# Optimization experiments

Measured on AMD Instinct MI355X. Metric: run time of the kernel, lower is better.

The kernel has to match this reference:

```python
import jax, jax.numpy as jnp
import numpy as np

N = 100000
E = 1600000
F_IN = 100
H = 64
C = 18
K = 2  # num_stacks
T = 2  # num_layers


def setup_inputs() -> dict:
    key = jax.random.key(0)
    ks = jax.random.split(key, 12)
    def glorot(k, shape):
        fan = shape[-2] + shape[-1]
        s = jnp.sqrt(6.0 / fan)
        return jax.random.uniform(k, shape, jnp.float32, -s, s)
    return {
        "x": jax.random.normal(ks[0], (N, F_IN), jnp.float32),
        "edge_index": jax.random.randint(ks[1], (2, E), 0, N, jnp.int64),
        "init_w1": glorot(ks[2], (K, F_IN, H)),
        "w1": glorot(ks[3], (K, H, H)),
        "root_w1": glorot(ks[4], (K, F_IN, H)),
        "b1": jnp.zeros((K, 1, H), jnp.float32),
        "init_w2": glorot(ks[5], (K, H, C)),
        "w2": glorot(ks[6], (K, C, C)),
        "root_w2": glorot(ks[7], (K, H, C)),
        "b2": jnp.zeros((K, 1, C), jnp.float32),
    }


def _gcn_norm(src, tgt):
    # symmetric normalization, no self loops (PyG ARMAConv default)
    deg = jax.ops.segment_sum(jnp.ones((E,), jnp.float32), tgt, num_segments=N)
    dis = jnp.where(deg > 0, jax.lax.rsqrt(jnp.maximum(deg, 1.0)), 0.0)
    return dis[src] * dis[tgt]  # [E]


def _arma_conv(x, src, tgt, norm, init_w, w, root_w, b):
    # x: [N, Fin]; returns [N, Fout]
    root = jnp.einsum('nf,kfh->knh', x, root_w)  # [K, N, Fout] (shared across layers)
    out = None
    for t in range(T):
        if t == 0:
            h = jnp.einsum('nf,kfh->knh', x, init_w)
        else:
            h = jnp.einsum('knh,khg->kng', out, w)
        # gather-scale-scatter propagation per stack
        msgs = h[:, src, :] * norm[None, :, None]  # [K, E, Fout]
        agg = jax.vmap(lambda m: jax.ops.segment_sum(m, tgt, num_segments=N))(msgs)
        out = jax.nn.relu(agg + root + b)
    return out.mean(axis=0)  # mean over stacks


def reference(x, edge_index, init_w1, w1, root_w1, b1, init_w2, w2, root_w2, b2):
    src, tgt = edge_index[0], edge_index[1]
    norm = _gcn_norm(src, tgt)
    h = jax.nn.relu(_arma_conv(x, src, tgt, norm, init_w1, w1, root_w1, b1))
    out = _arma_conv(h, src, tgt, norm, init_w2, w2, root_w2, b2)
    return jax.nn.log_softmax(out, axis=-1)
```

## Files before the change

### kernel.cpp

```cpp
#include <hip/hip_runtime.h>
#include <hip/hip_bf16.h>
#include <math.h>

#define N_NODES 100000
#define N_EDGES 1600000
#define F_IN 100
#define H 64
#define C 18
#define BSHIFT 8
#define BSIZE 256
#define NBUCKETS ((N_NODES + BSIZE - 1) >> BSHIFT)
#define NBLK 256
#define CHUNK (N_EDGES / NBLK)

typedef __attribute__((ext_vector_type(8))) short v8s;
typedef __attribute__((ext_vector_type(4))) float v4f;


__device__ __forceinline__ unsigned bf16_rne(float f) {
    unsigned u = __float_as_uint(f);
    return (u + 0x7FFFu + ((u >> 16) & 1u)) >> 16;
}
__device__ __forceinline__ unsigned pack_bf2(float a, float b) {
    return bf16_rne(a) | (bf16_rne(b) << 16);
}
__device__ __forceinline__ float2 unpack_bf2(unsigned u) {
    return make_float2(__uint_as_float(u << 16), __uint_as_float(u & 0xFFFF0000u));
}


__global__ void scan1_kernel(const int* __restrict__ cnt, int* __restrict__ excl,
                             int* __restrict__ bsum, int n) {
    __shared__ int tmp[256];
    int t = threadIdx.x;
    int i = blockIdx.x * 256 + t;
    int v = (i < n) ? cnt[i] : 0;
    tmp[t] = v;
    __syncthreads();
    for (int off = 1; off < 256; off <<= 1) {
        int xv = (t >= off) ? tmp[t - off] : 0;
        __syncthreads();
        tmp[t] += xv;
        __syncthreads();
    }
    if (i < n) excl[i] = tmp[t] - v;
    if (t == 255) bsum[blockIdx.x] = tmp[255];
}

__global__ void __launch_bounds__(512) scan2p_kernel(int* __restrict__ bsum, int nb) {
    __shared__ int s[512];
    int t = threadIdx.x;
    int v = (t < nb) ? bsum[t] : 0;
    s[t] = v;
    __syncthreads();
    for (int off = 1; off < 512; off <<= 1) {
        int xv = (t >= off) ? s[t - off] : 0;
        __syncthreads();
        s[t] += xv;
        __syncthreads();
    }
    if (t < nb) bsum[t] = s[t] - v;
}

__global__ void scan3_kernel(int* __restrict__ arr, const int* __restrict__ bsum,
                             int n, int sent) {
    int i = blockIdx.x * 256 + threadIdx.x;
    if (i < n) arr[i] += bsum[i >> 8];
    if (i == n && sent >= 0) arr[n] = sent;
}


__global__ void __launch_bounds__(256) histA_kernel(const int* __restrict__ tgt,
                                                    int* __restrict__ hist) {
    __shared__ int h[NBUCKETS];
    int blk = blockIdx.x, t = threadIdx.x;
    for (int i = t; i < NBUCKETS; i += 256) h[i] = 0;
    __syncthreads();
    int e0 = blk * CHUNK, e1 = e0 + CHUNK;
    for (int e = e0 + t; e < e1; e += 256) atomicAdd(&h[tgt[e] >> BSHIFT], 1);
    __syncthreads();
    for (int i = t; i < NBUCKETS; i += 256) hist[i * NBLK + blk] = h[i];
}

__global__ void __launch_bounds__(256) scatterC_kernel(
        const int* __restrict__ src, const int* __restrict__ tgt,
        const int* __restrict__ histx, unsigned* __restrict__ tmp) {
    __shared__ int cur[NBUCKETS];
    int blk = blockIdx.x, t = threadIdx.x;
    for (int i = t; i < NBUCKETS; i += 256) cur[i] = histx[i * NBLK + blk];
    __syncthreads();
    int e0 = blk * CHUNK, e1 = e0 + CHUNK;
    for (int e = e0 + t; e < e1; e += 256) {
        int s = src[e], tg = tgt[e];
        int b = tg >> BSHIFT;
        int pos = atomicAdd(&cur[b], 1);
        tmp[pos] = (unsigned)s | ((unsigned)(tg & (BSIZE - 1)) << 17);
    }
}

__global__ void __launch_bounds__(256) bucketD2_kernel(
        const unsigned* __restrict__ tmp, const int* __restrict__ histx,
        int* __restrict__ rp, float* __restrict__ dinv, int* __restrict__ ssrc) {
    __shared__ int cnt_l[BSIZE];
    __shared__ int scan_l[BSIZE];
    int b = blockIdx.x;
    int t = threadIdx.x;
    int e_lo = histx[(size_t)b * NBLK];
    int e_hi = (b + 1 < NBUCKETS) ? histx[(size_t)(b + 1) * NBLK] : N_EDGES;
    int n_lo = b << BSHIFT;
    int n_hi = min(n_lo + BSIZE, N_NODES);
    int nn = n_hi - n_lo;
    cnt_l[t] = 0;
    __syncthreads();
    for (int e = e_lo + t; e < e_hi; e += 256)
        atomicAdd(&cnt_l[(int)(tmp[e] >> 17)], 1);
    __syncthreads();
    int v = cnt_l[t];
    scan_l[t] = v;
    __syncthreads();
    for (int off = 1; off < 256; off <<= 1) {
        int xv = (t >= off) ? scan_l[t - off] : 0;
        __syncthreads();
        scan_l[t] += xv;
        __syncthreads();
    }
    int my_start = e_lo + scan_l[t] - v;
    if (t < nn) {
        rp[n_lo + t] = my_start;
        dinv[n_lo + t] = (v > 0) ? rsqrtf((float)v) : 0.f;
    }
    if (b == NBUCKETS - 1 && t == 0) rp[N_NODES] = N_EDGES;
    __syncthreads();
    cnt_l[t] = my_start;
    __syncthreads();
    for (int e = e_lo + t; e < e_hi; e += 256) {
        unsigned p = tmp[e];
        int s = (int)(p & 0x1FFFFu);
        int tl = (int)(p >> 17);
        int pos = atomicAdd(&cnt_l[tl], 1);
        ssrc[pos] = s;
    }
}


__global__ void __launch_bounds__(256) prep_w_kernel(
        const float* __restrict__ iw1, const float* __restrict__ rw1,
        const float* __restrict__ w1,  const float* __restrict__ iw2,
        const float* __restrict__ rw2, const float* __restrict__ w2,
        ushort* __restrict__ W1T, ushort* __restrict__ WmT,
        ushort* __restrict__ W2T, ushort* __restrict__ W3T) {
    int gid = blockIdx.x * 256 + threadIdx.x;
    if (gid < 32768) {
        int idx = gid;
        int m = idx >> 13, nn = (idx >> 7) & 63, kk = idx & 127;
        int stk = m & 1, isWr = m >> 1;
        float v = 0.f;
        if (kk < F_IN) v = (isWr ? rw1 : iw1)[((size_t)stk * F_IN + kk) * 64 + nn];
        W1T[idx] = (ushort)bf16_rne(v);
    } else if (gid < 32768 + 8192) {
        int idx = gid - 32768;
        int stk = idx >> 12, g = (idx >> 6) & 63, f = idx & 63;
        WmT[idx] = (ushort)bf16_rne(w1[((size_t)stk * 64 + f) * 64 + g]);
    } else if (gid < 32768 + 8192 + 8192) {
        int idx = gid - 32768 - 8192;
        int m = idx >> 11, col = (idx >> 6) & 31, k = idx & 63;
        int stk = m & 1, isWr = m >> 1;
        float v = 0.f;
        if (col < C) v = (isWr ? rw2 : iw2)[((size_t)stk * H + k) * C + col];
        W2T[idx] = (ushort)bf16_rne(v);
    } else if (gid < 32768 + 8192 + 8192 + 2048) {
        int idx = gid - 32768 - 8192 - 8192;
        int stk = idx >> 10, col = (idx >> 5) & 31, k = idx & 31;
        float v = 0.f;
        if (col < C && k < C) v = w2[((size_t)stk * C + k) * C + col];
        W3T[idx] = (ushort)bf16_rne(v);
    }
}


__global__ void __launch_bounds__(256) dense1_mfma(
        const float* __restrict__ x, const ushort* __restrict__ W1T,
        const float* __restrict__ dinv,
        unsigned* __restrict__ g, unsigned* __restrict__ root) {
    __shared__ char xs[64 * 256];
    int tid = threadIdx.x;
    int b0 = blockIdx.x * 64;
    for (int i = tid; i < 4096; i += 256) {
        int row = i >> 6, pr = i & 63;
        int grow = b0 + row;
        unsigned pv = 0;
        if (grow < N_NODES && 2 * pr < F_IN) {
            float v0 = x[(size_t)grow * F_IN + 2 * pr];
            float v1 = (2 * pr + 1 < F_IN) ? x[(size_t)grow * F_IN + 2 * pr + 1] : 0.f;
            pv = pack_bf2(v0, v1);
        }
        int gr = (pr >> 2) ^ (row & 7);
        *(unsigned*)(xs + row * 256 + (gr << 4) + (pr & 3) * 4) = pv;
    }
    __syncthreads();
    int lane = tid & 63;
    int w = __builtin_amdgcn_readfirstlane(tid >> 6);
    int q = lane >> 4, cl = lane & 15;
    int isWr = w >> 1;
    int colbase = (w & 1) * 32;
    v8s bfr[2][2][4];
    #pragma unroll
    for (int stk = 0; stk < 2; ++stk)
        #pragma unroll
        for (int nt = 0; nt < 2; ++nt)
            #pragma unroll
            for (int ks = 0; ks < 4; ++ks) {
                const ushort* p = W1T + ((size_t)(isWr * 2 + stk) * 64 + colbase + nt * 16 + cl) * 128
                                  + ks * 32 + q * 8;
                bfr[stk][nt][ks] = *(const v8s*)p;
            }
    #pragma unroll
    for (int mt = 0; mt < 4; ++mt) {
        v8s afr[4];
        #pragma unroll
        for (int ks = 0; ks < 4; ++ks) {
            int row = mt * 16 + cl;
            int gr = (ks * 4 + q) ^ (row & 7);
            afr[ks] = *(const v8s*)(xs + row * 256 + (gr << 4));
        }
        v4f acc[2][2];
        #pragma unroll
        for (int stk = 0; stk < 2; ++stk)
            #pragma unroll
            for (int nt = 0; nt < 2; ++nt) {
                v4f a = {0.f, 0.f, 0.f, 0.f};
                #pragma unroll
                for (int ks = 0; ks < 4; ++ks)
                    a = __builtin_amdgcn_mfma_f32_16x16x32_bf16(afr[ks], bfr[stk][nt][ks], a, 0, 0, 0);
                acc[stk][nt] = a;
            }
        #pragma unroll
        for (int nt = 0; nt < 2; ++nt)
            #pragma unroll
            for (int reg = 0; reg < 4; ++reg) {
                int node = b0 + mt * 16 + q * 4 + reg;
                if (node < N_NODES) {
                    int col = colbase + nt * 16 + cl;
                    if (isWr == 0) {
                        float dv = dinv[node];
                        g[(size_t)node * 64 + col] = pack_bf2(dv * acc[0][nt][reg], dv * acc[1][nt][reg]);
                    } else {
                        root[(size_t)node * 64 + col] = pack_bf2(acc[0][nt][reg], acc[1][nt][reg]);
                    }
                }
            }
    }
}

__global__ void __launch_bounds__(256) dense_mid_mfma(
        const ushort* __restrict__ hk0, const ushort* __restrict__ hk1,
        const ushort* __restrict__ WmT, const float* __restrict__ dinv,
        unsigned* __restrict__ g2) {
    __shared__ char hs[2 * 64 * 128];
    int tid = threadIdx.x;
    int b0 = blockIdx.x * 64;
    for (int i = tid; i < 1024; i += 256) {
        int stk = i >> 9, rem = i & 511, row = rem >> 3, gr = rem & 7;
        int grow = b0 + row;
        uint4 v = make_uint4(0, 0, 0, 0);
        const ushort* srcp = stk ? hk1 : hk0;
        if (grow < N_NODES) v = *(const uint4*)(srcp + (size_t)grow * 64 + gr * 8);
        *(uint4*)(hs + stk * 8192 + row * 128 + ((gr ^ (row & 7)) << 4)) = v;
    }
    __syncthreads();
    int lane = tid & 63;
    int w = __builtin_amdgcn_readfirstlane(tid >> 6);
    int q = lane >> 4, cl = lane & 15;
    v8s bfr[2][2];
    #pragma unroll
    for (int stk = 0; stk < 2; ++stk)
        #pragma unroll
        for (int ks = 0; ks < 2; ++ks)
            bfr[stk][ks] = *(const v8s*)(WmT + ((size_t)stk * 64 + w * 16 + cl) * 64 + ks * 32 + q * 8);
    #pragma unroll
    for (int mt = 0; mt < 4; ++mt) {
        v4f acc[2];
        #pragma unroll
        for (int stk = 0; stk < 2; ++stk) {
            v4f a = {0.f, 0.f, 0.f, 0.f};
            #pragma unroll
            for (int ks = 0; ks < 2; ++ks) {
                int row = mt * 16 + cl;
                int gr = (ks * 4 + q) ^ (row & 7);
                v8s af = *(const v8s*)(hs + stk * 8192 + row * 128 + (gr << 4));
                a = __builtin_amdgcn_mfma_f32_16x16x32_bf16(af, bfr[stk][ks], a, 0, 0, 0);
            }
            acc[stk] = a;
        }
        #pragma unroll
        for (int reg = 0; reg < 4; ++reg) {
            int node = b0 + mt * 16 + q * 4 + reg;
            if (node < N_NODES) {
                float dv = dinv[node];
                g2[(size_t)node * 64 + w * 16 + cl] = pack_bf2(dv * acc[0][reg], dv * acc[1][reg]);
            }
        }
    }
}

__global__ void __launch_bounds__(256) dense_y2_mfma(
        const ushort* __restrict__ yb, const ushort* __restrict__ W2T,
        const float* __restrict__ dinv,
        unsigned* __restrict__ h2, unsigned* __restrict__ root2) {
    __shared__ char ys[64 * 128];
    int tid = threadIdx.x;
    int b0 = blockIdx.x * 64;
    for (int i = tid; i < 512; i += 256) {
        int row = i >> 3, gr = i & 7;
        int grow = b0 + row;
        uint4 v = make_uint4(0, 0, 0, 0);
        if (grow < N_NODES) v = *(const uint4*)(yb + (size_t)grow * 64 + gr * 8);
        *(uint4*)(ys + row * 128 + ((gr ^ (row & 7)) << 4)) = v;
    }
    __syncthreads();
    int lane = tid & 63;
    int w = __builtin_amdgcn_readfirstlane(tid >> 6);
    int q = lane >> 4, cl = lane & 15;
    int isWr = w >> 1;
    int mbase = (w & 1) * 2;
    v8s bfr[2][2][2];
    #pragma unroll
    for (int stk = 0; stk < 2; ++stk)
        #pragma unroll
        for (int nt = 0; nt < 2; ++nt)
            #pragma unroll
            for (int ks = 0; ks < 2; ++ks)
                bfr[stk][nt][ks] = *(const v8s*)(W2T + ((size_t)(isWr * 2 + stk) * 32 + nt * 16 + cl) * 64
                                                 + ks * 32 + q * 8);
    #pragma unroll
    for (int mi = 0; mi < 2; ++mi) {
        int mt = mbase + mi;
        v8s afr[2];
        #pragma unroll
        for (int ks = 0; ks < 2; ++ks) {
            int row = mt * 16 + cl;
            int gr = (ks * 4 + q) ^ (row & 7);
            afr[ks] = *(const v8s*)(ys + row * 128 + (gr << 4));
        }
        v4f acc[2][2];
        #pragma unroll
        for (int stk = 0; stk < 2; ++stk)
            #pragma unroll
            for (int nt = 0; nt < 2; ++nt) {
                v4f a = {0.f, 0.f, 0.f, 0.f};
                #pragma unroll
                for (int ks = 0; ks < 2; ++ks)
                    a = __builtin_amdgcn_mfma_f32_16x16x32_bf16(afr[ks], bfr[stk][nt][ks], a, 0, 0, 0);
                acc[stk][nt] = a;
            }
        #pragma unroll
        for (int nt = 0; nt < 2; ++nt)
            #pragma unroll
            for (int reg = 0; reg < 4; ++reg) {
                int node = b0 + mt * 16 + q * 4 + reg;
                int col = nt * 16 + cl;
                if (node < N_NODES && col < C) {
                    if (isWr == 0) {
                        float dv = dinv[node];
                        h2[(size_t)node * C + col] = pack_bf2(dv * acc[0][nt][reg], dv * acc[1][nt][reg]);
                    } else {
                        root2[(size_t)node * C + col] = pack_bf2(acc[0][nt][reg], acc[1][nt][reg]);
                    }
                }
            }
    }
}

__global__ void __launch_bounds__(256) dense_last_mfma(
        const ushort* __restrict__ ok0, const ushort* __restrict__ ok1,
        const ushort* __restrict__ W3T, const float* __restrict__ dinv,
        unsigned* __restrict__ h3) {
    __shared__ char hs[2 * 64 * 64];
    int tid = threadIdx.x;
    int b0 = blockIdx.x * 64;
    for (int i = tid; i < 2048; i += 256) ((unsigned*)hs)[i] = 0;
    __syncthreads();
    for (int i = tid; i < 4096; i += 256) {
        int stk = i >> 11, row = (i >> 5) & 63, col = i & 31;
        int node = b0 + row;
        if (col < C && node < N_NODES) {
            ushort v = (stk ? ok1 : ok0)[(size_t)node * C + col];
            int gr = (col >> 3) ^ (row & 3);
            *(ushort*)(hs + stk * 4096 + row * 64 + (gr << 4) + (col & 7) * 2) = v;
        }
    }
    __syncthreads();
    int lane = tid & 63;
    int w = __builtin_amdgcn_readfirstlane(tid >> 6);
    int q = lane >> 4, cl = lane & 15;
    v8s bfr[2][2];
    #pragma unroll
    for (int stk = 0; stk < 2; ++stk)
        #pragma unroll
        for (int nt = 0; nt < 2; ++nt)
            bfr[stk][nt] = *(const v8s*)(W3T + ((size_t)stk * 32 + nt * 16 + cl) * 32 + q * 8);
    int row = w * 16 + cl;
    int gr = q ^ (row & 3);
    v8s af0 = *(const v8s*)(hs + row * 64 + (gr << 4));
    v8s af1 = *(const v8s*)(hs + 4096 + row * 64 + (gr << 4));
    v4f acc[2][2];
    #pragma unroll
    for (int nt = 0; nt < 2; ++nt) {
        acc[0][nt] = __builtin_amdgcn_mfma_f32_16x16x32_bf16(af0, bfr[0][nt], (v4f){0.f,0.f,0.f,0.f}, 0, 0, 0);
        acc[1][nt] = __builtin_amdgcn_mfma_f32_16x16x32_bf16(af1, bfr[1][nt], (v4f){0.f,0.f,0.f,0.f}, 0, 0, 0);
    }
    #pragma unroll
    for (int nt = 0; nt < 2; ++nt)
        #pragma unroll
        for (int reg = 0; reg < 4; ++reg) {
            int node = b0 + w * 16 + q * 4 + reg;
            int col = nt * 16 + cl;
            if (node < N_NODES && col < C) {
                float dv = dinv[node];
                h3[(size_t)node * C + col] = pack_bf2(dv * acc[0][nt][reg], dv * acc[1][nt][reg]);
            }
        }
}


template <int FINAL>
__global__ void __launch_bounds__(256) prop64_kernel(
        const unsigned* __restrict__ g, const unsigned* __restrict__ root,
        const float* __restrict__ b, const float* __restrict__ dinv,
        const int* __restrict__ rp, const int* __restrict__ ssrc,
        ushort* __restrict__ ok0, ushort* __restrict__ ok1, ushort* __restrict__ yb) {
    int lane = threadIdx.x & 63;
    int wid = __builtin_amdgcn_readfirstlane((int)((blockIdx.x * 256 + threadIdx.x) >> 6));
    if (wid >= N_NODES) return;
    int e0 = rp[wid], e1 = rp[wid + 1];
    float a0 = 0.f, a1 = 0.f;
    int e = e0;
    for (; e + 8 <= e1; e += 8) {
        unsigned u[8];
        #pragma unroll
        for (int j = 0; j < 8; ++j) u[j] = g[(size_t)ssrc[e + j] * H + lane];
        #pragma unroll
        for (int j = 0; j < 8; ++j) { float2 v = unpack_bf2(u[j]); a0 += v.x; a1 += v.y; }
    }
    for (; e < e1; ++e) {
        float2 v = unpack_bf2(g[(size_t)ssrc[e] * H + lane]);
        a0 += v.x; a1 += v.y;
    }
    float dv = dinv[wid];
    float2 rt = unpack_bf2(root[(size_t)wid * H + lane]);
    float o0 = fmaxf(fmaf(dv, a0, rt.x + b[lane]), 0.f);
    float o1 = fmaxf(fmaf(dv, a1, rt.y + b[H + lane]), 0.f);
    if (FINAL) {
        yb[(size_t)wid * H + lane] = (ushort)bf16_rne(0.5f * (o0 + o1));
    } else {
        ok0[(size_t)wid * H + lane] = (ushort)bf16_rne(o0);
        ok1[(size_t)wid * H + lane] = (ushort)bf16_rne(o1);
    }
}

template <int FINAL>
__global__ void __launch_bounds__(256) prop18_kernel(
        const unsigned* __restrict__ g, const unsigned* __restrict__ root,
        const float* __restrict__ b, const float* __restrict__ dinv,
        const int* __restrict__ rp, const int* __restrict__ ssrc,
        ushort* __restrict__ ok0, ushort* __restrict__ ok1, float* __restrict__ outp) {
    int lane = threadIdx.x & 63;
    int wid = __builtin_amdgcn_readfirstlane((int)((blockIdx.x * 256 + threadIdx.x) >> 6));
    if (wid >= N_NODES) return;
    int e0 = rp[wid], e1 = rp[wid + 1];
    bool act = lane < C;
    int c = act ? lane : 0;
    float a0 = 0.f, a1 = 0.f;
    int e = e0;
    for (; e + 8 <= e1; e += 8) {
        unsigned u[8];
        #pragma unroll
        for (int j = 0; j < 8; ++j) u[j] = g[(size_t)ssrc[e + j] * C + c];
        if (act) {
            #pragma unroll
            for (int j = 0; j < 8; ++j) { float2 v = unpack_bf2(u[j]); a0 += v.x; a1 += v.y; }
        }
    }
    for (; e < e1; ++e) {
        float2 v = unpack_bf2(g[(size_t)ssrc[e] * C + c]);
        if (act) { a0 += v.x; a1 += v.y; }
    }
    float dv = dinv[wid];
    if (!FINAL) {
        if (act) {
            float2 rt = unpack_bf2(root[(size_t)wid * C + c]);
            float o0 = fmaxf(fmaf(dv, a0, rt.x + b[c]), 0.f);
            float o1 = fmaxf(fmaf(dv, a1, rt.y + b[C + c]), 0.f);
            ok0[(size_t)wid * C + c] = (ushort)bf16_rne(o0);
            ok1[(size_t)wid * C + c] = (ushort)bf16_rne(o1);
        }
    } else {
        float m = -INFINITY;
        if (act) {
            float2 rt = unpack_bf2(root[(size_t)wid * C + c]);
            float o0 = fmaxf(fmaf(dv, a0, rt.x + b[c]), 0.f);
            float o1 = fmaxf(fmaf(dv, a1, rt.y + b[C + c]), 0.f);
            m = 0.5f * (o0 + o1);
        }
        float mx = m;
        #pragma unroll
        for (int off = 16; off >= 1; off >>= 1) mx = fmaxf(mx, __shfl_xor(mx, off, 64));
        float ex = act ? __expf(m - mx) : 0.f;
        float sum = ex;
        #pragma unroll
        for (int off = 16; off >= 1; off >>= 1) sum += __shfl_xor(sum, off, 64);
        if (act) outp[(size_t)wid * C + c] = m - mx - logf(sum);
    }
}


extern "C" void kernel_launch(void* const* d_in, const int* in_sizes, int n_in,
                              void* d_out, int out_size, void* d_ws, size_t ws_size,
                              hipStream_t stream) {
    const float* x        = (const float*)d_in[0];
    const int*   ei       = (const int*)d_in[1];
    const float* init_w1  = (const float*)d_in[2];
    const float* w1       = (const float*)d_in[3];
    const float* root_w1  = (const float*)d_in[4];
    const float* b1       = (const float*)d_in[5];
    const float* init_w2  = (const float*)d_in[6];
    const float* w2       = (const float*)d_in[7];
    const float* root_w2  = (const float*)d_in[8];
    const float* b2       = (const float*)d_in[9];
    const int* src = ei;
    const int* tgt = ei + N_EDGES;
    float* out = (float*)d_out;

    char* w = (char*)d_ws;
    size_t off = 0;
    auto alloc = [&](size_t bytes) -> char* {
        char* p = w + off;
        off += (bytes + 255) & ~(size_t)255;
        return p;
    };
    int*      rp    = (int*)alloc((size_t)(N_NODES + 1) * 4);
    float*    dinv  = (float*)alloc((size_t)N_NODES * 4);
    int*      bsum  = (int*)alloc(512 * 4);
    int*      hist  = (int*)alloc((size_t)NBUCKETS * NBLK * 4);
    int*      histx = (int*)alloc((size_t)NBUCKETS * NBLK * 4);
    unsigned* tmp   = (unsigned*)alloc((size_t)N_EDGES * 4);
    int*      ssrc  = (int*)alloc((size_t)N_EDGES * 4);
    ushort*   W1T   = (ushort*)alloc((size_t)4 * 64 * 128 * 2);
    ushort*   WmT   = (ushort*)alloc((size_t)2 * 64 * 64 * 2);
    ushort*   W2T   = (ushort*)alloc((size_t)4 * 32 * 64 * 2);
    ushort*   W3T   = (ushort*)alloc((size_t)2 * 32 * 32 * 2);
    unsigned* g1    = (unsigned*)alloc((size_t)N_NODES * H * 4);
    unsigned* root1 = (unsigned*)alloc((size_t)N_NODES * H * 4);
    ushort*   hk0   = (ushort*)alloc((size_t)N_NODES * H * 2);
    ushort*   hk1   = (ushort*)alloc((size_t)N_NODES * H * 2);
    unsigned* g2    = (unsigned*)alloc((size_t)N_NODES * H * 4);
    ushort*   yb    = (ushort*)alloc((size_t)N_NODES * H * 2);
    unsigned* h2u    = g1;
    unsigned* root2u = g1 + (size_t)N_NODES * C;
    unsigned* h3u    = g1 + (size_t)2 * N_NODES * C;
    ushort*   p18k0  = (ushort*)root1;
    ushort*   p18k1  = (ushort*)root1 + (size_t)N_NODES * C;

    int nbH = (NBUCKETS * NBLK + 255) / 256;

    histA_kernel<<<NBLK, 256, 0, stream>>>(tgt, hist);
    scan1_kernel<<<nbH, 256, 0, stream>>>(hist, histx, bsum, NBUCKETS * NBLK);
    scan2p_kernel<<<1, 512, 0, stream>>>(bsum, nbH);
    scan3_kernel<<<nbH, 256, 0, stream>>>(histx, bsum, NBUCKETS * NBLK, -1);
    scatterC_kernel<<<NBLK, 256, 0, stream>>>(src, tgt, histx, tmp);
    bucketD2_kernel<<<NBUCKETS, 256, 0, stream>>>(tmp, histx, rp, dinv, ssrc);

    prep_w_kernel<<<200, 256, 0, stream>>>(init_w1, root_w1, w1, init_w2, root_w2, w2,
                                           W1T, WmT, W2T, W3T);

    int gblocks = (N_NODES + 63) / 64;
    int pgrid   = (N_NODES + 3) / 4;

    dense1_mfma<<<gblocks, 256, 0, stream>>>(x, W1T, dinv, g1, root1);
    prop64_kernel<0><<<pgrid, 256, 0, stream>>>(g1, root1, b1, dinv, rp, ssrc, hk0, hk1, nullptr);
    dense_mid_mfma<<<gblocks, 256, 0, stream>>>(hk0, hk1, WmT, dinv, g2);
    prop64_kernel<1><<<pgrid, 256, 0, stream>>>(g2, root1, b1, dinv, rp, ssrc, nullptr, nullptr, yb);

    dense_y2_mfma<<<gblocks, 256, 0, stream>>>(yb, W2T, dinv, h2u, root2u);
    prop18_kernel<0><<<pgrid, 256, 0, stream>>>(h2u, root2u, b2, dinv, rp, ssrc, p18k0, p18k1, nullptr);
    dense_last_mfma<<<gblocks, 256, 0, stream>>>(p18k0, p18k1, W3T, dinv, h3u);
    prop18_kernel<1><<<pgrid, 256, 0, stream>>>(h3u, root2u, b2, dinv, rp, ssrc, nullptr, nullptr, out);
}
```

Measured before the change: 358.6 us.

## Use nontemporal loads/stores, fuse scan2 with weight prep, drop scan3 pass

Marks streaming loads and stores across the CSR build, dense MFMA and propagation kernels as nontemporal, to reduce cache pollution so the randomly gathered feature rows stay resident. Merges the single-block block-sum scan into the weight-prep launch and removes the scan3 add pass by folding the block offsets into the consumers (scatterC and bucketD2). This cuts two kernel launches and one pass over the histogram, at the cost of extra bsum reads and possible cache bypass on data that is reused later (rp, root, the dense outputs read by prop).

```diff
diff --git a/kernel.cpp b/kernel.cpp
--- a/kernel.cpp
+++ b/kernel.cpp
@@ -16,6 +16,9 @@
 typedef __attribute__((ext_vector_type(8))) short v8s;
 typedef __attribute__((ext_vector_type(4))) float v4f;
 
+#define NTL(p) __builtin_nontemporal_load(p)
+#define NTS(v, p) __builtin_nontemporal_store(v, p)
+
 
 __device__ __forceinline__ unsigned bf16_rne(float f) {
     unsigned u = __float_as_uint(f);
@@ -34,7 +37,7 @@
     __shared__ int tmp[256];
     int t = threadIdx.x;
     int i = blockIdx.x * 256 + t;
-    int v = (i < n) ? cnt[i] : 0;
+    int v = (i < n) ? NTL(&cnt[i]) : 0;
     tmp[t] = v;
     __syncthreads();
     for (int off = 1; off < 256; off <<= 1) {
@@ -43,113 +46,33 @@
         tmp[t] += xv;
         __syncthreads();
     }
-    if (i < n) excl[i] = tmp[t] - v;
+    if (i < n) NTS(tmp[t] - v, &excl[i]);
     if (t == 255) bsum[blockIdx.x] = tmp[255];
 }
 
-__global__ void __launch_bounds__(512) scan2p_kernel(int* __restrict__ bsum, int nb) {
-    __shared__ int s[512];
-    int t = threadIdx.x;
-    int v = (t < nb) ? bsum[t] : 0;
-    s[t] = v;
-    __syncthreads();
-    for (int off = 1; off < 512; off <<= 1) {
-        int xv = (t >= off) ? s[t - off] : 0;
-        __syncthreads();
-        s[t] += xv;
-        __syncthreads();
-    }
-    if (t < nb) bsum[t] = s[t] - v;
-}
-
-__global__ void scan3_kernel(int* __restrict__ arr, const int* __restrict__ bsum,
-                             int n, int sent) {
-    int i = blockIdx.x * 256 + threadIdx.x;
-    if (i < n) arr[i] += bsum[i >> 8];
-    if (i == n && sent >= 0) arr[n] = sent;
-}
-
-
-__global__ void __launch_bounds__(256) histA_kernel(const int* __restrict__ tgt,
-                                                    int* __restrict__ hist) {
-    __shared__ int h[NBUCKETS];
-    int blk = blockIdx.x, t = threadIdx.x;
-    for (int i = t; i < NBUCKETS; i += 256) h[i] = 0;
-    __syncthreads();
-    int e0 = blk * CHUNK, e1 = e0 + CHUNK;
-    for (int e = e0 + t; e < e1; e += 256) atomicAdd(&h[tgt[e] >> BSHIFT], 1);
-    __syncthreads();
-    for (int i = t; i < NBUCKETS; i += 256) hist[i * NBLK + blk] = h[i];
-}
-
-__global__ void __launch_bounds__(256) scatterC_kernel(
-        const int* __restrict__ src, const int* __restrict__ tgt,
-        const int* __restrict__ histx, unsigned* __restrict__ tmp) {
-    __shared__ int cur[NBUCKETS];
-    int blk = blockIdx.x, t = threadIdx.x;
-    for (int i = t; i < NBUCKETS; i += 256) cur[i] = histx[i * NBLK + blk];
-    __syncthreads();
-    int e0 = blk * CHUNK, e1 = e0 + CHUNK;
-    for (int e = e0 + t; e < e1; e += 256) {
-        int s = src[e], tg = tgt[e];
-        int b = tg >> BSHIFT;
-        int pos = atomicAdd(&cur[b], 1);
-        tmp[pos] = (unsigned)s | ((unsigned)(tg & (BSIZE - 1)) << 17);
-    }
-}
-
-__global__ void __launch_bounds__(256) bucketD2_kernel(
-        const unsigned* __restrict__ tmp, const int* __restrict__ histx,
-        int* __restrict__ rp, float* __restrict__ dinv, int* __restrict__ ssrc) {
-    __shared__ int cnt_l[BSIZE];
-    __shared__ int scan_l[BSIZE];
-    int b = blockIdx.x;
-    int t = threadIdx.x;
-    int e_lo = histx[(size_t)b * NBLK];
-    int e_hi = (b + 1 < NBUCKETS) ? histx[(size_t)(b + 1) * NBLK] : N_EDGES;
-    int n_lo = b << BSHIFT;
-    int n_hi = min(n_lo + BSIZE, N_NODES);
-    int nn = n_hi - n_lo;
-    cnt_l[t] = 0;
-    __syncthreads();
-    for (int e = e_lo + t; e < e_hi; e += 256)
-        atomicAdd(&cnt_l[(int)(tmp[e] >> 17)], 1);
-    __syncthreads();
-    int v = cnt_l[t];
-    scan_l[t] = v;
-    __syncthreads();
-    for (int off = 1; off < 256; off <<= 1) {
-        int xv = (t >= off) ? scan_l[t - off] : 0;
-        __syncthreads();
-        scan_l[t] += xv;
-        __syncthreads();
-    }
-    int my_start = e_lo + scan_l[t] - v;
-    if (t < nn) {
-        rp[n_lo + t] = my_start;
-        dinv[n_lo + t] = (v > 0) ? rsqrtf((float)v) : 0.f;
-    }
-    if (b == NBUCKETS - 1 && t == 0) rp[N_NODES] = N_EDGES;
-    __syncthreads();
-    cnt_l[t] = my_start;
-    __syncthreads();
-    for (int e = e_lo + t; e < e_hi; e += 256) {
-        unsigned p = tmp[e];
-        int s = (int)(p & 0x1FFFFu);
-        int tl = (int)(p >> 17);
-        int pos = atomicAdd(&cnt_l[tl], 1);
-        ssrc[pos] = s;
-    }
-}
-
-
-__global__ void __launch_bounds__(256) prep_w_kernel(
+__global__ void __launch_bounds__(512) scan2p_prep_kernel(
+        int* __restrict__ bsum, int nb,
         const float* __restrict__ iw1, const float* __restrict__ rw1,
         const float* __restrict__ w1,  const float* __restrict__ iw2,
         const float* __restrict__ rw2, const float* __restrict__ w2,
         ushort* __restrict__ W1T, ushort* __restrict__ WmT,
         ushort* __restrict__ W2T, ushort* __restrict__ W3T) {
-    int gid = blockIdx.x * 256 + threadIdx.x;
+    int t = threadIdx.x;
+    if (blockIdx.x == 0) {
+        __shared__ int s[512];
+        int v = (t < nb) ? bsum[t] : 0;
+        s[t] = v;
+        __syncthreads();
+        for (int off = 1; off < 512; off <<= 1) {
+            int xv = (t >= off) ? s[t - off] : 0;
+            __syncthreads();
+            s[t] += xv;
+            __syncthreads();
+        }
+        if (t < nb) bsum[t] = s[t] - v;
+        return;
+    }
+    int gid = (blockIdx.x - 1) * 512 + t;
     if (gid < 32768) {
         int idx = gid;
         int m = idx >> 13, nn = (idx >> 7) & 63, kk = idx & 127;
@@ -178,6 +101,89 @@
 }
 
 
+__global__ void __launch_bounds__(256) histA_kernel(const int* __restrict__ tgt,
+                                                    int* __restrict__ hist) {
+    __shared__ int h[NBUCKETS];
+    int blk = blockIdx.x, t = threadIdx.x;
+    for (int i = t; i < NBUCKETS; i += 256) h[i] = 0;
+    __syncthreads();
+    int e0 = blk * CHUNK, e1 = e0 + CHUNK;
+    for (int e = e0 + t; e < e1; e += 256) atomicAdd(&h[NTL(&tgt[e]) >> BSHIFT], 1);
+    __syncthreads();
+    for (int i = t; i < NBUCKETS; i += 256) NTS(h[i], &hist[i * NBLK + blk]);
+}
+
+__global__ void __launch_bounds__(256) scatterC_kernel(
+        const int* __restrict__ src, const int* __restrict__ tgt,
+        const int* __restrict__ histx, const int* __restrict__ bsum,
+        unsigned* __restrict__ tmp) {
+    __shared__ int cur[NBUCKETS];
+    int blk = blockIdx.x, t = threadIdx.x;
+    for (int i = t; i < NBUCKETS; i += 256) {
+        int gi = i * NBLK + blk;
+        cur[i] = histx[gi] + bsum[gi >> 8];
+    }
+    __syncthreads();
+    int e0 = blk * CHUNK, e1 = e0 + CHUNK;
+    for (int e = e0 + t; e < e1; e += 256) {
+        int s = NTL(&src[e]), tg = NTL(&tgt[e]);
+        int b = tg >> BSHIFT;
+        int pos = atomicAdd(&cur[b], 1);
+        NTS((unsigned)s | ((unsigned)(tg & (BSIZE - 1)) << 17), &tmp[pos]);
+    }
+}
+
+__global__ void __launch_bounds__(256) bucketD2_kernel(
+        const unsigned* __restrict__ tmp, const int* __restrict__ histx,
+        const int* __restrict__ bsum,
+        int* __restrict__ rp, float* __restrict__ dinv, int* __restrict__ ssrc) {
+    __shared__ int cnt_l[BSIZE];
+    __shared__ int scan_l[BSIZE];
+    int b = blockIdx.x;
+    int t = threadIdx.x;
+    int gi_lo = b * NBLK;
+    int e_lo = histx[gi_lo] + bsum[gi_lo >> 8];
+    int e_hi = N_EDGES;
+    if (b + 1 < NBUCKETS) {
+        int gi_hi = (b + 1) * NBLK;
+        e_hi = histx[gi_hi] + bsum[gi_hi >> 8];
+    }
+    int n_lo = b << BSHIFT;
+    int n_hi = min(n_lo + BSIZE, N_NODES);
+    int nn = n_hi - n_lo;
+    cnt_l[t] = 0;
+    __syncthreads();
+    for (int e = e_lo + t; e < e_hi; e += 256)
+        atomicAdd(&cnt_l[(int)(NTL(&tmp[e]) >> 17)], 1);
+    __syncthreads();
+    int v = cnt_l[t];
+    scan_l[t] = v;
+    __syncthreads();
+    for (int off = 1; off < 256; off <<= 1) {
+        int xv = (t >= off) ? scan_l[t - off] : 0;
+        __syncthreads();
+        scan_l[t] += xv;
+        __syncthreads();
+    }
+    int my_start = e_lo + scan_l[t] - v;
+    if (t < nn) {
+        NTS(my_start, &rp[n_lo + t]);
+        NTS((v > 0) ? rsqrtf((float)v) : 0.f, &dinv[n_lo + t]);
+    }
+    if (b == NBUCKETS - 1 && t == 0) rp[N_NODES] = N_EDGES;
+    __syncthreads();
+    cnt_l[t] = my_start;
+    __syncthreads();
+    for (int e = e_lo + t; e < e_hi; e += 256) {
+        unsigned p = NTL(&tmp[e]);
+        int s = (int)(p & 0x1FFFFu);
+        int tl = (int)(p >> 17);
+        int pos = atomicAdd(&cnt_l[tl], 1);
+        NTS(s, &ssrc[pos]);
+    }
+}
+
+
 __global__ void __launch_bounds__(256) dense1_mfma(
         const float* __restrict__ x, const ushort* __restrict__ W1T,
         const float* __restrict__ dinv,
@@ -190,8 +196,8 @@
         int grow = b0 + row;
         unsigned pv = 0;
         if (grow < N_NODES && 2 * pr < F_IN) {
-            float v0 = x[(size_t)grow * F_IN + 2 * pr];
-            float v1 = (2 * pr + 1 < F_IN) ? x[(size_t)grow * F_IN + 2 * pr + 1] : 0.f;
+            float v0 = NTL(&x[(size_t)grow * F_IN + 2 * pr]);
+            float v1 = (2 * pr + 1 < F_IN) ? NTL(&x[(size_t)grow * F_IN + 2 * pr + 1]) : 0.f;
             pv = pack_bf2(v0, v1);
         }
         int gr = (pr >> 2) ^ (row & 7);
@@ -243,9 +249,11 @@
                     int col = colbase + nt * 16 + cl;
                     if (isWr == 0) {
                         float dv = dinv[node];
-                        g[(size_t)node * 64 + col] = pack_bf2(dv * acc[0][nt][reg], dv * acc[1][nt][reg]);
+                        NTS(pack_bf2(dv * acc[0][nt][reg], dv * acc[1][nt][reg]),
+                            &g[(size_t)node * 64 + col]);
                     } else {
-                        root[(size_t)node * 64 + col] = pack_bf2(acc[0][nt][reg], acc[1][nt][reg]);
+                        NTS(pack_bf2(acc[0][nt][reg], acc[1][nt][reg]),
+                            &root[(size_t)node * 64 + col]);
                     }
                 }
             }
@@ -297,7 +305,8 @@
             int node = b0 + mt * 16 + q * 4 + reg;
             if (node < N_NODES) {
                 float dv = dinv[node];
-                g2[(size_t)node * 64 + w * 16 + cl] = pack_bf2(dv * acc[0][reg], dv * acc[1][reg]);
+                NTS(pack_bf2(dv * acc[0][reg], dv * acc[1][reg]),
+                    &g2[(size_t)node * 64 + w * 16 + cl]);
             }
         }
     }
@@ -362,9 +371,11 @@
                 if (node < N_NODES && col < C) {
                     if (isWr == 0) {
                         float dv = dinv[node];
-                        h2[(size_t)node * C + col] = pack_bf2(dv * acc[0][nt][reg], dv * acc[1][nt][reg]);
+                        NTS(pack_bf2(dv * acc[0][nt][reg], dv * acc[1][nt][reg]),
+                            &h2[(size_t)node * C + col]);
                     } else {
-                        root2[(size_t)node * C + col] = pack_bf2(acc[0][nt][reg], acc[1][nt][reg]);
+                        NTS(pack_bf2(acc[0][nt][reg], acc[1][nt][reg]),
+                            &root2[(size_t)node * C + col]);
                     }
                 }
             }
@@ -384,7 +395,7 @@
         int stk = i >> 11, row = (i >> 5) & 63, col = i & 31;
         int node = b0 + row;
         if (col < C && node < N_NODES) {
-            ushort v = (stk ? ok1 : ok0)[(size_t)node * C + col];
+            ushort v = NTL(&(stk ? ok1 : ok0)[(size_t)node * C + col]);
             int gr = (col >> 3) ^ (row & 3);
             *(ushort*)(hs + stk * 4096 + row * 64 + (gr << 4) + (col & 7) * 2) = v;
         }
@@ -417,7 +428,8 @@
             int col = nt * 16 + cl;
             if (node < N_NODES && col < C) {
                 float dv = dinv[node];
-                h3[(size_t)node * C + col] = pack_bf2(dv * acc[0][nt][reg], dv * acc[1][nt][reg]);
+                NTS(pack_bf2(dv * acc[0][nt][reg], dv * acc[1][nt][reg]),
+                    &h3[(size_t)node * C + col]);
             }
         }
 }
@@ -432,29 +444,32 @@
     int lane = threadIdx.x & 63;
     int wid = __builtin_amdgcn_readfirstlane((int)((blockIdx.x * 256 + threadIdx.x) >> 6));
     if (wid >= N_NODES) return;
-    int e0 = rp[wid], e1 = rp[wid + 1];
+    int e0 = NTL(&rp[wid]), e1 = NTL(&rp[wid + 1]);
     float a0 = 0.f, a1 = 0.f;
     int e = e0;
     for (; e + 8 <= e1; e += 8) {
         unsigned u[8];
-        #pragma unroll
-        for (int j = 0; j < 8; ++j) u[j] = g[(size_t)ssrc[e + j] * H + lane];
+        int s[8];
+        #pragma unroll
+        for (int j = 0; j < 8; ++j) s[j] = NTL(&ssrc[e + j]);
+        #pragma unroll
+        for (int j = 0; j < 8; ++j) u[j] = g[(size_t)s[j] * H + lane];
         #pragma unroll
         for (int j = 0; j < 8; ++j) { float2 v = unpack_bf2(u[j]); a0 += v.x; a1 += v.y; }
     }
     for (; e < e1; ++e) {
-        float2 v = unpack_bf2(g[(size_t)ssrc[e] * H + lane]);
+        float2 v = unpack_bf2(g[(size_t)NTL(&ssrc[e]) * H + lane]);
         a0 += v.x; a1 += v.y;
     }
     float dv = dinv[wid];
-    float2 rt = unpack_bf2(root[(size_t)wid * H + lane]);
+    float2 rt = unpack_bf2(NTL(&root[(size_t)wid * H + lane]));
     float o0 = fmaxf(fmaf(dv, a0, rt.x + b[lane]), 0.f);
     float o1 = fmaxf(fmaf(dv, a1, rt.y + b[H + lane]), 0.f);
     if (FINAL) {
-        yb[(size_t)wid * H + lane] = (ushort)bf16_rne(0.5f * (o0 + o1));
+        NTS((ushort)bf16_rne(0.5f * (o0 + o1)), &yb[(size_t)wid * H + lane]);
     } else {
-        ok0[(size_t)wid * H + lane] = (ushort)bf16_rne(o0);
-        ok1[(size_t)wid * H + lane] = (ushort)bf16_rne(o1);
+        NTS((ushort)bf16_rne(o0), &ok0[(size_t)wid * H + lane]);
+        NTS((ushort)bf16_rne(o1), &ok1[(size_t)wid * H + lane]);
     }
 }
 
@@ -467,37 +482,40 @@
     int lane = threadIdx.x & 63;
     int wid = __builtin_amdgcn_readfirstlane((int)((blockIdx.x * 256 + threadIdx.x) >> 6));
     if (wid >= N_NODES) return;
-    int e0 = rp[wid], e1 = rp[wid + 1];
+    int e0 = NTL(&rp[wid]), e1 = NTL(&rp[wid + 1]);
     bool act = lane < C;
     int c = act ? lane : 0;
     float a0 = 0.f, a1 = 0.f;
     int e = e0;
     for (; e + 8 <= e1; e += 8) {
         unsigned u[8];
-        #pragma unroll
-        for (int j = 0; j < 8; ++j) u[j] = g[(size_t)ssrc[e + j] * C + c];
+        int s[8];
+        #pragma unroll
+        for (int j = 0; j < 8; ++j) s[j] = NTL(&ssrc[e + j]);
+        #pragma unroll
+        for (int j = 0; j < 8; ++j) u[j] = g[(size_t)s[j] * C + c];
         if (act) {
             #pragma unroll
             for (int j = 0; j < 8; ++j) { float2 v = unpack_bf2(u[j]); a0 += v.x; a1 += v.y; }
         }
     }
     for (; e < e1; ++e) {
-        float2 v = unpack_bf2(g[(size_t)ssrc[e] * C + c]);
+        float2 v = unpack_bf2(g[(size_t)NTL(&ssrc[e]) * C + c]);
         if (act) { a0 += v.x; a1 += v.y; }
     }
     float dv = dinv[wid];
     if (!FINAL) {
         if (act) {
-            float2 rt = unpack_bf2(root[(size_t)wid * C + c]);
+            float2 rt = unpack_bf2(NTL(&root[(size_t)wid * C + c]));
             float o0 = fmaxf(fmaf(dv, a0, rt.x + b[c]), 0.f);
             float o1 = fmaxf(fmaf(dv, a1, rt.y + b[C + c]), 0.f);
-            ok0[(size_t)wid * C + c] = (ushort)bf16_rne(o0);
-            ok1[(size_t)wid * C + c] = (ushort)bf16_rne(o1);
+            NTS((ushort)bf16_rne(o0), &ok0[(size_t)wid * C + c]);
+            NTS((ushort)bf16_rne(o1), &ok1[(size_t)wid * C + c]);
         }
     } else {
         float m = -INFINITY;
         if (act) {
-            float2 rt = unpack_bf2(root[(size_t)wid * C + c]);
+            float2 rt = unpack_bf2(NTL(&root[(size_t)wid * C + c]));
             float o0 = fmaxf(fmaf(dv, a0, rt.x + b[c]), 0.f);
             float o1 = fmaxf(fmaf(dv, a1, rt.y + b[C + c]), 0.f);
             m = 0.5f * (o0 + o1);
@@ -509,7 +527,7 @@
         float sum = ex;
         #pragma unroll
         for (int off = 16; off >= 1; off >>= 1) sum += __shfl_xor(sum, off, 64);
-        if (act) outp[(size_t)wid * C + c] = m - mx - logf(sum);
+        if (act) NTS(m - mx - logf(sum), &outp[(size_t)wid * C + c]);
     }
 }
 
@@ -565,13 +583,11 @@
 
     histA_kernel<<<NBLK, 256, 0, stream>>>(tgt, hist);
     scan1_kernel<<<nbH, 256, 0, stream>>>(hist, histx, bsum, NBUCKETS * NBLK);
-    scan2p_kernel<<<1, 512, 0, stream>>>(bsum, nbH);
-    scan3_kernel<<<nbH, 256, 0, stream>>>(histx, bsum, NBUCKETS * NBLK, -1);
-    scatterC_kernel<<<NBLK, 256, 0, stream>>>(src, tgt, histx, tmp);
-    bucketD2_kernel<<<NBUCKETS, 256, 0, stream>>>(tmp, histx, rp, dinv, ssrc);
-
-    prep_w_kernel<<<200, 256, 0, stream>>>(init_w1, root_w1, w1, init_w2, root_w2, w2,
-                                           W1T, WmT, W2T, W3T);
+    scan2p_prep_kernel<<<101, 512, 0, stream>>>(bsum, nbH,
+                                                init_w1, root_w1, w1, init_w2, root_w2, w2,
+                                                W1T, WmT, W2T, W3T);
+    scatterC_kernel<<<NBLK, 256, 0, stream>>>(src, tgt, histx, bsum, tmp);
+    bucketD2_kernel<<<NBUCKETS, 256, 0, stream>>>(tmp, histx, bsum, rp, dinv, ssrc);
 
     int gblocks = (N_NODES + 63) / 64;
     int pgrid   = (N_NODES + 3) / 4;
```

Result: slower. 483.4 us (+34.8%).
